# Performance work log

Measured on AMD Instinct MI355X. Metric: run time of the kernel, lower is better.

## Reference

```python
import jax, jax.numpy as jnp
import numpy as np

B, T, D, H = 16, 256, 128, 256  # batch, max_len, input_size, hidden_size (= attention hidden)


def _gru(x_seq, h0, Wih, Whh, bih, bhh):
    """Torch-style GRU over time. x_seq: [B,T,H_in], h0: [B,H]. Returns outputs [B,T,H], hT [B,H]."""
    x_proj = jnp.einsum('bti,gi->btg', x_seq, Wih) + bih  # [B,T,3H], precompute input projections

    def step(h, xp):
        gi_r, gi_z, gi_n = jnp.split(xp, 3, axis=-1)
        gh = h @ Whh.T + bhh
        gh_r, gh_z, gh_n = jnp.split(gh, 3, axis=-1)
        r = jax.nn.sigmoid(gi_r + gh_r)
        z = jax.nn.sigmoid(gi_z + gh_z)
        n = jnp.tanh(gi_n + r * gh_n)
        h_new = (1.0 - z) * n + z * h
        return h_new, h_new

    hT, outs = jax.lax.scan(step, h0, jnp.swapaxes(x_proj, 0, 1))  # scan over time
    return jnp.swapaxes(outs, 0, 1), hT


def setup_inputs() -> dict:
    key = jax.random.key(0)
    ks = jax.random.split(key, 16)
    s = lambda fan: 1.0 / np.sqrt(fan)
    inp = {
        'inputs': jax.random.normal(ks[0], (B, T, D), dtype=jnp.float32),
        'targets': jax.vmap(lambda k: jax.random.permutation(k, T))(jax.random.split(ks[1], B)).astype(jnp.int64),
        'W_enc': jax.random.normal(ks[2], (H, D), dtype=jnp.float32) * s(D),
        'b_enc': jnp.zeros((H,), dtype=jnp.float32),
        'enc_Wih': jax.random.normal(ks[3], (3 * H, H), dtype=jnp.float32) * s(H),
        'enc_Whh': jax.random.normal(ks[4], (3 * H, H), dtype=jnp.float32) * s(H),
        'enc_bih': jnp.zeros((3 * H,), dtype=jnp.float32),
        'enc_bhh': jnp.zeros((3 * H,), dtype=jnp.float32),
        'dec_Wih': jax.random.normal(ks[5], (3 * H, H), dtype=jnp.float32) * s(H),
        'dec_Whh': jax.random.normal(ks[6], (3 * H, H), dtype=jnp.float32) * s(H),
        'dec_bih': jnp.zeros((3 * H,), dtype=jnp.float32),
        'dec_bhh': jnp.zeros((3 * H,), dtype=jnp.float32),
        'Wq': jax.random.normal(ks[7], (H, H), dtype=jnp.float32) * s(H),
        'Wk': jax.random.normal(ks[8], (H, H), dtype=jnp.float32) * s(H),
        'v': jax.random.normal(ks[9], (H,), dtype=jnp.float32) * s(H),
    }
    return inp


def reference(inputs, targets, W_enc, b_enc, enc_Wih, enc_Whh, enc_bih, enc_bhh,
              dec_Wih, dec_Whh, dec_bih, dec_bhh, Wq, Wk, v):
    # encoder_linear (dropout = 0 at inference)
    enc_in = jnp.einsum('btd,hd->bth', inputs, W_enc) + b_enc  # [B,T,H]
    enc_out, hT = _gru(enc_in, jnp.zeros((B, H), dtype=inputs.dtype), enc_Wih, enc_Whh, enc_bih, enc_bhh)
    # teacher forcing: decoder inputs are encoder_inputs gathered at rolled targets
    dec_idx = jnp.roll(targets, 1, axis=1)  # [B,T]
    dec_rnn_in = jnp.take_along_axis(enc_in, dec_idx[:, :, None], axis=1)  # [B,T,H]
    dec_out, _ = _gru(dec_rnn_in, hT, dec_Wih, dec_Whh, dec_bih, dec_bhh)  # [B,T,H]
    # steps mask: position j available at step t iff j not in targets[:, :t]
    onehot = jax.nn.one_hot(targets, T, dtype=jnp.int32)         # [B,T,T]
    prev = jnp.cumsum(onehot, axis=1) - onehot                   # exclusive cumsum
    steps_mask = prev == 0                                       # [B,T(query),T(key)] bool
    # Bahdanau additive attention: v . tanh(Wq q + Wk k)
    q = jnp.einsum('bth,ah->bta', dec_out, Wq)  # [B,T,A]
    k = jnp.einsum('bsh,ah->bsa', enc_out, Wk)  # [B,S,A]
    scores = jnp.einsum('btsa,a->bts', jnp.tanh(q[:, :, None, :] + k[:, None, :, :]), v)  # [B,T,S]
    logits = jnp.where(steps_mask, scores, jnp.float32(-1e9))
    return logits
```

## Files before the change

kernel.cpp:

```cpp
#include <hip/hip_runtime.h>
#include <hip/hip_fp16.h>

#define B_ 16
#define T_ 256
#define D_ 128
#define H_ 256

typedef _Float16 f16;
typedef __attribute__((ext_vector_type(2))) _Float16 f16x2;
typedef __attribute__((ext_vector_type(4))) int i32x4;

__device__ __forceinline__ float fast_rcp(float x) {
#if __has_builtin(__builtin_amdgcn_rcpf)
    return __builtin_amdgcn_rcpf(x);
#else
    return 1.0f / x;
#endif
}
__device__ __forceinline__ float sigmoid_f(float x) {
    return fast_rcp(1.0f + __expf(-x));
}
__device__ __forceinline__ float tanh_f(float x) {
    float e = __expf(2.0f * x);
    return 1.0f - 2.0f * fast_rcp(1.0f + e);
}
__device__ __forceinline__ float tanh_pade(float x) {
    x = fminf(4.f, fmaxf(-4.f, x));
    float x2 = x * x;
    return x * (27.f + x2) * fast_rcp(27.f + 9.f * x2);
}
__device__ __forceinline__ int dot8(int a, int b, int c) {
#if __has_builtin(__builtin_amdgcn_sdot8)
    return __builtin_amdgcn_sdot8(a, b, c, false);
#else
    int d;
    asm("v_dot8_i32_i4 %0, %1, %2, %3" : "=v"(d) : "v"(a), "v"(b), "v"(c));
    return d;
#endif
}
template <int CTRL>
__device__ __forceinline__ int dpp_quad(int x) {
    return __builtin_amdgcn_update_dpp(0, x, CTRL, 0xF, 0xF, true);
}
#define DPP_XOR1 0xB1
#define DPP_XOR2 0x4E

__global__ __launch_bounds__(256) void k_wprep4(const float* __restrict__ wa,
                                                const float* __restrict__ wb,
                                                int* __restrict__ w4a, int* __restrict__ w4b,
                                                float* __restrict__ sca, float* __restrict__ scb) {
    int wid = blockIdx.x * 4 + (threadIdx.x >> 6);
    int l = threadIdx.x & 63;
    const float* W = wid < 768 ? wa : wb;
    int* w4 = wid < 768 ? w4a : w4b;
    float* sc = wid < 768 ? sca : scb;
    int r = wid & 767;
    int g = r >> 8, j = r & 255;
    const float* Wr = W + r * 256;
    float v[8];
    float m = 0.f;
    if (l < 32) {
#pragma unroll
        for (int q = 0; q < 8; ++q) {
            v[q] = Wr[8 * l + q];
            m = fmaxf(m, fabsf(v[q]));
        }
    }
#pragma unroll
    for (int d = 1; d < 64; d <<= 1) m = fmaxf(m, __shfl_xor(m, d));
    float qs = m > 0.f ? 7.f / m : 0.f;
    if (l == 0) sc[r] = m / 49.f;
    if (l < 32) {
        int pk = 0;
#pragma unroll
        for (int q = 0; q < 8; ++q) pk |= ((int)rintf(v[q] * qs) & 15) << (4 * q);
        int hf = l >> 4, i = l & 15;
        w4[(j * 2 + hf) * 48 + g * 16 + i] = pk;
    }
}

__global__ void k_pos(const int* __restrict__ tgt, int* __restrict__ pos) {
    __shared__ int pl[256];
    int b = blockIdx.x, tid = threadIdx.x;
    pl[tid] = T_;
    __syncthreads();
    atomicMin(&pl[tgt[b * 256 + tid] & 255], tid);
    __syncthreads();
    pos[b * 256 + tid] = pl[tid];
}

__global__ __launch_bounds__(256) void k_proj3(const float* __restrict__ inputs,
                                               const float* __restrict__ Wenc,
                                               const float* __restrict__ benc,
                                               const float* __restrict__ We,
                                               const float* __restrict__ bihe,
                                               const float* __restrict__ bhhe,
                                               const float* __restrict__ Wd,
                                               const float* __restrict__ bihd,
                                               const float* __restrict__ bhhd,
                                               const int* __restrict__ tgt,
                                               f16x2* __restrict__ giAe,
                                               f16* __restrict__ giBe,
                                               f16x2* __restrict__ giAd,
                                               f16* __restrict__ giBd) {
    __shared__ float s_in[16][128];
    __shared__ float s_enc[16][256];
    int blk = blockIdx.x;
    bool isdec = blk >= 256;
    int bt0 = (blk & 255) * 16;
    int b = bt0 >> 8;
    int a = threadIdx.x;
    const float* W = isdec ? Wd : We;
    const float* bih = isdec ? bihd : bihe;
    const float* bhh = isdec ? bhhd : bhhe;
    f16x2* giA = isdec ? giAd : giAe;
    f16* giB = isdec ? giBd : giBe;

    int tsrc[16];
#pragma unroll
    for (int tt = 0; tt < 16; ++tt) {
        int t = (bt0 & 255) + tt;
        tsrc[tt] = isdec ? (tgt[(b << 8) + ((t + 255) & 255)] & 255) : t;
    }
#pragma unroll
    for (int it = 0; it < 2; ++it) {
        int idx = a + it * 256;
        int row = idx >> 5, k4 = idx & 31;
        ((float4*)s_in[row])[k4] =
            *(const float4*)(inputs + (b * 256 + tsrc[row]) * 128 + k4 * 4);
    }
    __syncthreads();
    {
        float eacc[16];
#pragma unroll
        for (int tt = 0; tt < 16; ++tt) eacc[tt] = benc[a];
        const float* wr = Wenc + a * 128;
        for (int k = 0; k < 128; k += 4) {
            float4 w4 = *(const float4*)(wr + k);
#pragma unroll
            for (int tt = 0; tt < 16; ++tt) {
                float4 x4 = *(const float4*)&s_in[tt][k];
                eacc[tt] += w4.x * x4.x + w4.y * x4.y + w4.z * x4.z + w4.w * x4.w;
            }
        }
#pragma unroll
        for (int tt = 0; tt < 16; ++tt) s_enc[tt][a] = eacc[tt];
    }
    __syncthreads();
    float acc0[16], acc1[16], acc2[16];
    float b0 = bih[a] + bhh[a];
    float b1 = bih[a + 256] + bhh[a + 256];
    float b2 = bih[a + 512];
#pragma unroll
    for (int tt = 0; tt < 16; ++tt) { acc0[tt] = b0; acc1[tt] = b1; acc2[tt] = b2; }
    const float* w0 = W + a * H_;
    const float* w1 = W + (a + 256) * H_;
    const float* w2 = W + (a + 512) * H_;
    for (int k = 0; k < H_; k += 4) {
        float4 a4 = *(const float4*)(w0 + k);
        float4 b4 = *(const float4*)(w1 + k);
        float4 c4 = *(const float4*)(w2 + k);
#pragma unroll
        for (int tt = 0; tt < 16; ++tt) {
            float4 x4 = *(const float4*)&s_enc[tt][k];
            acc0[tt] += a4.x * x4.x + a4.y * x4.y + a4.z * x4.z + a4.w * x4.w;
            acc1[tt] += b4.x * x4.x + b4.y * x4.y + b4.z * x4.z + b4.w * x4.w;
            acc2[tt] += c4.x * x4.x + c4.y * x4.y + c4.z * x4.z + c4.w * x4.w;
        }
    }
#pragma unroll
    for (int tt = 0; tt < 16; ++tt) {
        int row = bt0 + tt;
        giA[row * 256 + a] = (f16x2){(f16)acc0[tt], (f16)acc1[tt]};
        giB[row * 256 + a] = (f16)acc2[tt];
    }
}

__global__ __launch_bounds__(512)
__attribute__((amdgpu_waves_per_eu(2, 2)))
void k_gru2(const int* __restrict__ w4e, const int* __restrict__ w4d,
            const float* __restrict__ sce, const float* __restrict__ scd,
            const f16x2* __restrict__ giAe, const f16* __restrict__ giBe,
            const f16x2* __restrict__ giAd, const f16* __restrict__ giBd,
            const float* __restrict__ bhhe, const float* __restrict__ bhhd,
            float* __restrict__ enc_out, float* __restrict__ dec_out) {
    __shared__ __align__(16) int sh_h4[2][32];
    const int tid = threadIdx.x;
    const int m = blockIdx.x;
    const int j = tid >> 1;
    const int hf = tid & 1;

    if (tid < 64) ((int*)sh_h4)[tid] = 0;
    float hj = 0.f;
    __syncthreads();

    for (int ph = 0; ph < 2; ++ph) {
        const int* w4 = ph ? w4d : w4e;
        const float* scp = ph ? scd : sce;
        const float sc0 = scp[j], sc1 = scp[256 + j], sc2 = scp[512 + j];
        const float bn = (ph ? bhhd : bhhe)[512 + j];
        const f16x2* gA = (ph ? giAd : giAe) + m * (T_ * 256);
        const f16* gB = (ph ? giBd : giBe) + m * (T_ * 256);
        float* outp = (ph ? dec_out : enc_out) + m * (T_ * H_);

        i32x4 wq[3][4];
        {
            unsigned long long base = (unsigned long long)(w4 + tid * 48);
#pragma unroll
            for (int g = 0; g < 3; ++g)
#pragma unroll
                for (int q4 = 0; q4 < 4; ++q4)
                    asm volatile("global_load_dwordx4 %0, %1, off offset:%2"
                                 : "=v"(wq[g][q4]) : "v"(base), "i"(g * 64 + q4 * 16));
            asm volatile("s_waitcnt vmcnt(0)" ::: "memory");
        }

        f16x2 gab = gA[j];
        f16 gn = gB[j];

        for (int t = 0; t < T_; ++t) {
            const int cur = t & 1;
            int a0 = 0, a1 = 0, a2 = 0;
            const i32x4* hb = (const i32x4*)((const char*)sh_h4 + cur * 128 + hf * 64);
#pragma unroll
            for (int q4 = 0; q4 < 4; ++q4) {
                i32x4 h4 = hb[q4];
#pragma unroll
                for (int d = 0; d < 4; ++d) {
                    a0 = dot8(wq[0][q4][d], h4[d], a0);
                    a1 = dot8(wq[1][q4][d], h4[d], a1);
                    a2 = dot8(wq[2][q4][d], h4[d], a2);
                }
            }
            const int tn = (t < T_ - 1) ? t + 1 : t;
            f16x2 ngab = gA[tn * 256 + j];
            f16 ngn = gB[tn * 256 + j];

            a0 += dpp_quad<DPP_XOR1>(a0);
            a1 += dpp_quad<DPP_XOR1>(a1);
            a2 += dpp_quad<DPP_XOR1>(a2);
            float p0 = (float)a0 * sc0;
            float p1 = (float)a1 * sc1;
            float p2 = (float)a2 * sc2;

            float rr = sigmoid_f((float)gab[0] + p0);
            float zz = sigmoid_f((float)gab[1] + p1);
            float nv = tanh_f((float)gn + rr * (p2 + bn));
            float hn = (1.f - zz) * nv + zz * hj;
            hj = hn;

            if (hf) outp[t * H_ + j] = hn;
            int nib = (int)rintf(hn * 7.f) & 15;
            int hi = dpp_quad<DPP_XOR2>(nib);
            if ((tid & 3) == 0)
                ((char*)sh_h4)[(cur ^ 1) * 128 + (tid >> 2)] = (char)(nib | (hi << 4));

            gab = ngab; gn = ngn;
            asm volatile("s_waitcnt lgkmcnt(0)" ::: "memory");
            __builtin_amdgcn_s_barrier();
        }
    }
}

__global__ __launch_bounds__(256) void k_qk(const float* __restrict__ dec_out,
                                            const float* __restrict__ Wq,
                                            const float* __restrict__ enc_out,
                                            const float* __restrict__ Wk,
                                            float* __restrict__ q,
                                            float* __restrict__ kT) {
    __shared__ float tile[8][256];
    int blk = blockIdx.x;
    bool isq = blk < 512;
    int bt0 = (isq ? blk : blk - 512) * 8;
    const float* in = isq ? dec_out : enc_out;
    const float* W = isq ? Wq : Wk;
    int a = threadIdx.x;
    float acc[8];
#pragma unroll
    for (int tt = 0; tt < 8; ++tt) acc[tt] = 0.f;
    const float* w0 = W + a * H_;
    for (int k = 0; k < H_; k += 4) {
        float4 w4 = *(const float4*)(w0 + k);
#pragma unroll
        for (int tt = 0; tt < 8; ++tt) {
            float4 x4 = *(const float4*)(in + (bt0 + tt) * H_ + k);
            acc[tt] += w4.x * x4.x + w4.y * x4.y + w4.z * x4.z + w4.w * x4.w;
        }
    }
    if (isq) {
#pragma unroll
        for (int tt = 0; tt < 8; ++tt) q[(bt0 + tt) * H_ + a] = acc[tt];
    } else {
#pragma unroll
        for (int tt = 0; tt < 8; ++tt) tile[tt][a] = acc[tt];
        __syncthreads();
        int b = bt0 >> 8, s0 = bt0 & 255;
        float4 f0 = {tile[0][a], tile[1][a], tile[2][a], tile[3][a]};
        float4 f1 = {tile[4][a], tile[5][a], tile[6][a], tile[7][a]};
        *(float4*)(kT + b * (T_ * H_) + a * T_ + s0) = f0;
        *(float4*)(kT + b * (T_ * H_) + a * T_ + s0 + 4) = f1;
    }
}

__global__ __launch_bounds__(256) void k_scores(const float* __restrict__ q,
                                                const float* __restrict__ kT,
                                                const float* __restrict__ v,
                                                const int* __restrict__ pos,
                                                float* __restrict__ out) {
    __shared__ float sq[4][256];
    __shared__ float sv[256];
    int blk = blockIdx.x;
    int b = blk >> 6;
    int t0 = (blk & 63) * 4;
    int s = threadIdx.x;
    sv[s] = v[s];
#pragma unroll
    for (int tt = 0; tt < 4; ++tt)
        sq[tt][s] = q[((b << 8) + t0 + tt) * H_ + s];
    __syncthreads();
    int ps = pos[(b << 8) + s];
    float acc[4] = {0.f, 0.f, 0.f, 0.f};
    const float* kTb = kT + b * (T_ * H_);
    for (int a = 0; a < H_; ++a) {
        float kv = kTb[a * T_ + s];
        float va = sv[a];
#pragma unroll
        for (int tt = 0; tt < 4; ++tt) {
            float th = tanh_pade(sq[tt][a] + kv);
            acc[tt] += va * th;
        }
    }
#pragma unroll
    for (int tt = 0; tt < 4; ++tt) {
        int t = t0 + tt;
        out[((b << 8) + t) * T_ + s] = (t <= ps) ? acc[tt] : -1.0e9f;
    }
}

extern "C" void kernel_launch(void* const* d_in, const int* in_sizes, int n_in,
                              void* d_out, int out_size, void* d_ws, size_t ws_size,
                              hipStream_t stream) {
    (void)in_sizes; (void)n_in; (void)out_size; (void)ws_size;
    const float* inputs   = (const float*)d_in[0];
    const int* targets    = (const int*)d_in[1];
    const float* W_enc   = (const float*)d_in[2];
    const float* b_enc   = (const float*)d_in[3];
    const float* enc_Wih = (const float*)d_in[4];
    const float* enc_Whh = (const float*)d_in[5];
    const float* enc_bih = (const float*)d_in[6];
    const float* enc_bhh = (const float*)d_in[7];
    const float* dec_Wih = (const float*)d_in[8];
    const float* dec_Whh = (const float*)d_in[9];
    const float* dec_bih = (const float*)d_in[10];
    const float* dec_bhh = (const float*)d_in[11];
    const float* Wq = (const float*)d_in[12];
    const float* Wk = (const float*)d_in[13];
    const float* v  = (const float*)d_in[14];
    float* out = (float*)d_out;

    float* ws = (float*)d_ws;
    f16x2* giAe    = (f16x2*)ws;
    f16*   giBe    = (f16*)(ws + 1048576);
    f16x2* giAd    = (f16x2*)(ws + 1572864);
    f16*   giBd    = (f16*)(ws + 2621440);
    float* enc_out = ws + 3145728;
    float* dec_out = ws + 4194304;
    int*   w4e     = (int*)(ws + 5242880);
    int*   w4d     = (int*)(ws + 5292032);
    float* sce     = ws + 5341184;
    float* scd     = ws + 5341952;
    int*   pos     = (int*)(ws + 5342720);
    float* q  = (float*)giAe;
    float* kT = (float*)giAd;

    k_wprep4<<<384, 256, 0, stream>>>(enc_Whh, dec_Whh, w4e, w4d, sce, scd);
    k_pos<<<16, 256, 0, stream>>>(targets, pos);
    k_proj3<<<512, 256, 0, stream>>>(inputs, W_enc, b_enc,
                                     enc_Wih, enc_bih, enc_bhh,
                                     dec_Wih, dec_bih, dec_bhh,
                                     targets, giAe, giBe, giAd, giBd);
    k_gru2<<<16, 512, 0, stream>>>(w4e, w4d, sce, scd, giAe, giBe, giAd, giBd,
                                   enc_bhh, dec_bhh, enc_out, dec_out);
    k_qk<<<1024, 256, 0, stream>>>(dec_out, Wq, enc_out, Wk, q, kT);
    k_scores<<<1024, 256, 0, stream>>>(q, kT, v, pos, out);
}
```

Before: 473.5 us.

## Merge prep kernels into one launch and fuse Q projection into scores

Folds weight quantization, target-position computation and input projections into a single kernel using block-index ranges, which cuts two launches. The Q projection moves into the scores kernel, so q is computed from dec_out held in shared memory and is no longer written to and read back from global memory. The K projection keeps its own kernel. The tanh clamp now uses a single med3 instruction. The cost is a larger shared-memory footprint in the scores kernel and more per-block compute there.

```diff
diff --git a/kernel.cpp b/kernel.cpp
--- a/kernel.cpp
+++ b/kernel.cpp
@@ -25,7 +25,11 @@
     return 1.0f - 2.0f * fast_rcp(1.0f + e);
 }
 __device__ __forceinline__ float tanh_pade(float x) {
+#if __has_builtin(__builtin_amdgcn_fmed3f)
+    x = __builtin_amdgcn_fmed3f(x, -4.f, 4.f);
+#else
     x = fminf(4.f, fmaxf(-4.f, x));
+#endif
     float x2 = x * x;
     return x * (27.f + x2) * fast_rcp(27.f + 9.f * x2);
 }
@@ -45,71 +49,68 @@
 #define DPP_XOR1 0xB1
 #define DPP_XOR2 0x4E
 
-__global__ __launch_bounds__(256) void k_wprep4(const float* __restrict__ wa,
-                                                const float* __restrict__ wb,
-                                                int* __restrict__ w4a, int* __restrict__ w4b,
-                                                float* __restrict__ sca, float* __restrict__ scb) {
-    int wid = blockIdx.x * 4 + (threadIdx.x >> 6);
-    int l = threadIdx.x & 63;
-    const float* W = wid < 768 ? wa : wb;
-    int* w4 = wid < 768 ? w4a : w4b;
-    float* sc = wid < 768 ? sca : scb;
-    int r = wid & 767;
-    int g = r >> 8, j = r & 255;
-    const float* Wr = W + r * 256;
-    float v[8];
-    float m = 0.f;
-    if (l < 32) {
-#pragma unroll
-        for (int q = 0; q < 8; ++q) {
-            v[q] = Wr[8 * l + q];
-            m = fmaxf(m, fabsf(v[q]));
-        }
-    }
-#pragma unroll
-    for (int d = 1; d < 64; d <<= 1) m = fmaxf(m, __shfl_xor(m, d));
-    float qs = m > 0.f ? 7.f / m : 0.f;
-    if (l == 0) sc[r] = m / 49.f;
-    if (l < 32) {
-        int pk = 0;
-#pragma unroll
-        for (int q = 0; q < 8; ++q) pk |= ((int)rintf(v[q] * qs) & 15) << (4 * q);
-        int hf = l >> 4, i = l & 15;
-        w4[(j * 2 + hf) * 48 + g * 16 + i] = pk;
-    }
-}
-
-__global__ void k_pos(const int* __restrict__ tgt, int* __restrict__ pos) {
-    __shared__ int pl[256];
-    int b = blockIdx.x, tid = threadIdx.x;
-    pl[tid] = T_;
-    __syncthreads();
-    atomicMin(&pl[tgt[b * 256 + tid] & 255], tid);
-    __syncthreads();
-    pos[b * 256 + tid] = pl[tid];
-}
-
-__global__ __launch_bounds__(256) void k_proj3(const float* __restrict__ inputs,
-                                               const float* __restrict__ Wenc,
-                                               const float* __restrict__ benc,
-                                               const float* __restrict__ We,
-                                               const float* __restrict__ bihe,
-                                               const float* __restrict__ bhhe,
-                                               const float* __restrict__ Wd,
-                                               const float* __restrict__ bihd,
-                                               const float* __restrict__ bhhd,
-                                               const int* __restrict__ tgt,
-                                               f16x2* __restrict__ giAe,
-                                               f16* __restrict__ giBe,
-                                               f16x2* __restrict__ giAd,
-                                               f16* __restrict__ giBd) {
+__global__ __launch_bounds__(256)
+void k_prep_proj(const float* __restrict__ wa, const float* __restrict__ wb,
+                 int* __restrict__ w4a, int* __restrict__ w4b,
+                 float* __restrict__ sca, float* __restrict__ scb,
+                 const int* __restrict__ tgt, int* __restrict__ pos,
+                 const float* __restrict__ inputs,
+                 const float* __restrict__ Wenc, const float* __restrict__ benc,
+                 const float* __restrict__ We, const float* __restrict__ bihe,
+                 const float* __restrict__ bhhe,
+                 const float* __restrict__ Wd, const float* __restrict__ bihd,
+                 const float* __restrict__ bhhd,
+                 f16x2* __restrict__ giAe, f16* __restrict__ giBe,
+                 f16x2* __restrict__ giAd, f16* __restrict__ giBd) {
+    int blk = blockIdx.x;
+    int a = threadIdx.x;
+    if (blk < 384) {
+        int wid = blk * 4 + (a >> 6);
+        int l = a & 63;
+        const float* W = wid < 768 ? wa : wb;
+        int* w4 = wid < 768 ? w4a : w4b;
+        float* sc = wid < 768 ? sca : scb;
+        int r = wid & 767;
+        int g = r >> 8, j = r & 255;
+        const float* Wr = W + r * 256;
+        float v[8];
+        float m = 0.f;
+        if (l < 32) {
+#pragma unroll
+            for (int q = 0; q < 8; ++q) {
+                v[q] = Wr[8 * l + q];
+                m = fmaxf(m, fabsf(v[q]));
+            }
+        }
+#pragma unroll
+        for (int d = 1; d < 64; d <<= 1) m = fmaxf(m, __shfl_xor(m, d));
+        float qs = m > 0.f ? 7.f / m : 0.f;
+        if (l == 0) sc[r] = m / 49.f;
+        if (l < 32) {
+            int pk = 0;
+#pragma unroll
+            for (int q = 0; q < 8; ++q) pk |= ((int)rintf(v[q] * qs) & 15) << (4 * q);
+            int hf = l >> 4, i = l & 15;
+            w4[(j * 2 + hf) * 48 + g * 16 + i] = pk;
+        }
+        return;
+    }
+    if (blk < 400) {
+        __shared__ int pl[256];
+        int b = blk - 384;
+        pl[a] = T_;
+        __syncthreads();
+        atomicMin(&pl[tgt[b * 256 + a] & 255], a);
+        __syncthreads();
+        pos[b * 256 + a] = pl[a];
+        return;
+    }
     __shared__ float s_in[16][128];
     __shared__ float s_enc[16][256];
-    int blk = blockIdx.x;
-    bool isdec = blk >= 256;
-    int bt0 = (blk & 255) * 16;
+    int pblk = blk - 400;
+    bool isdec = pblk >= 256;
+    int bt0 = (pblk & 255) * 16;
     int b = bt0 >> 8;
-    int a = threadIdx.x;
     const float* W = isdec ? Wd : We;
     const float* bih = isdec ? bihd : bihe;
     const float* bhh = isdec ? bhhd : bhhe;
@@ -262,51 +263,41 @@
     }
 }
 
-__global__ __launch_bounds__(256) void k_qk(const float* __restrict__ dec_out,
-                                            const float* __restrict__ Wq,
-                                            const float* __restrict__ enc_out,
+__global__ __launch_bounds__(256) void k_kT(const float* __restrict__ enc_out,
                                             const float* __restrict__ Wk,
-                                            float* __restrict__ q,
                                             float* __restrict__ kT) {
     __shared__ float tile[8][256];
-    int blk = blockIdx.x;
-    bool isq = blk < 512;
-    int bt0 = (isq ? blk : blk - 512) * 8;
-    const float* in = isq ? dec_out : enc_out;
-    const float* W = isq ? Wq : Wk;
+    int bt0 = blockIdx.x * 8;
     int a = threadIdx.x;
     float acc[8];
 #pragma unroll
     for (int tt = 0; tt < 8; ++tt) acc[tt] = 0.f;
-    const float* w0 = W + a * H_;
+    const float* w0 = Wk + a * H_;
     for (int k = 0; k < H_; k += 4) {
         float4 w4 = *(const float4*)(w0 + k);
 #pragma unroll
         for (int tt = 0; tt < 8; ++tt) {
-            float4 x4 = *(const float4*)(in + (bt0 + tt) * H_ + k);
+            float4 x4 = *(const float4*)(enc_out + (bt0 + tt) * H_ + k);
             acc[tt] += w4.x * x4.x + w4.y * x4.y + w4.z * x4.z + w4.w * x4.w;
         }
     }
-    if (isq) {
-#pragma unroll
-        for (int tt = 0; tt < 8; ++tt) q[(bt0 + tt) * H_ + a] = acc[tt];
-    } else {
-#pragma unroll
-        for (int tt = 0; tt < 8; ++tt) tile[tt][a] = acc[tt];
-        __syncthreads();
-        int b = bt0 >> 8, s0 = bt0 & 255;
-        float4 f0 = {tile[0][a], tile[1][a], tile[2][a], tile[3][a]};
-        float4 f1 = {tile[4][a], tile[5][a], tile[6][a], tile[7][a]};
-        *(float4*)(kT + b * (T_ * H_) + a * T_ + s0) = f0;
-        *(float4*)(kT + b * (T_ * H_) + a * T_ + s0 + 4) = f1;
-    }
-}
-
-__global__ __launch_bounds__(256) void k_scores(const float* __restrict__ q,
+#pragma unroll
+    for (int tt = 0; tt < 8; ++tt) tile[tt][a] = acc[tt];
+    __syncthreads();
+    int b = bt0 >> 8, s0 = bt0 & 255;
+    float4 f0 = {tile[0][a], tile[1][a], tile[2][a], tile[3][a]};
+    float4 f1 = {tile[4][a], tile[5][a], tile[6][a], tile[7][a]};
+    *(float4*)(kT + b * (T_ * H_) + a * T_ + s0) = f0;
+    *(float4*)(kT + b * (T_ * H_) + a * T_ + s0 + 4) = f1;
+}
+
+__global__ __launch_bounds__(256) void k_scores(const float* __restrict__ dec_out,
+                                                const float* __restrict__ Wq,
                                                 const float* __restrict__ kT,
                                                 const float* __restrict__ v,
                                                 const int* __restrict__ pos,
                                                 float* __restrict__ out) {
+    __shared__ float sdec[4][256];
     __shared__ float sq[4][256];
     __shared__ float sv[256];
     int blk = blockIdx.x;
@@ -316,7 +307,22 @@
     sv[s] = v[s];
 #pragma unroll
     for (int tt = 0; tt < 4; ++tt)
-        sq[tt][s] = q[((b << 8) + t0 + tt) * H_ + s];
+        sdec[tt][s] = dec_out[((b << 8) + t0 + tt) * H_ + s];
+    __syncthreads();
+    {
+        float qa[4] = {0.f, 0.f, 0.f, 0.f};
+        const float* wq = Wq + s * H_;
+        for (int k = 0; k < H_; k += 4) {
+            float4 w4 = *(const float4*)(wq + k);
+#pragma unroll
+            for (int tt = 0; tt < 4; ++tt) {
+                float4 x4 = *(const float4*)&sdec[tt][k];
+                qa[tt] += w4.x * x4.x + w4.y * x4.y + w4.z * x4.z + w4.w * x4.w;
+            }
+        }
+#pragma unroll
+        for (int tt = 0; tt < 4; ++tt) sq[tt][s] = qa[tt];
+    }
     __syncthreads();
     int ps = pos[(b << 8) + s];
     float acc[4] = {0.f, 0.f, 0.f, 0.f};
@@ -370,17 +376,15 @@
     float* sce     = ws + 5341184;
     float* scd     = ws + 5341952;
     int*   pos     = (int*)(ws + 5342720);
-    float* q  = (float*)giAe;
     float* kT = (float*)giAd;
 
-    k_wprep4<<<384, 256, 0, stream>>>(enc_Whh, dec_Whh, w4e, w4d, sce, scd);
-    k_pos<<<16, 256, 0, stream>>>(targets, pos);
-    k_proj3<<<512, 256, 0, stream>>>(inputs, W_enc, b_enc,
-                                     enc_Wih, enc_bih, enc_bhh,
-                                     dec_Wih, dec_bih, dec_bhh,
-                                     targets, giAe, giBe, giAd, giBd);
+    k_prep_proj<<<912, 256, 0, stream>>>(enc_Whh, dec_Whh, w4e, w4d, sce, scd,
+                                         targets, pos, inputs, W_enc, b_enc,
+                                         enc_Wih, enc_bih, enc_bhh,
+                                         dec_Wih, dec_bih, dec_bhh,
+                                         giAe, giBe, giAd, giBd);
     k_gru2<<<16, 512, 0, stream>>>(w4e, w4d, sce, scd, giAe, giBe, giAd, giBd,
                                    enc_bhh, dec_bhh, enc_out, dec_out);
-    k_qk<<<1024, 256, 0, stream>>>(dec_out, Wq, enc_out, Wk, q, kT);
-    k_scores<<<1024, 256, 0, stream>>>(q, kT, v, pos, out);
-}
+    k_kT<<<512, 256, 0, stream>>>(enc_out, Wk, kT);
+    k_scores<<<1024, 256, 0, stream>>>(dec_out, Wq, kT, v, pos, out);
+}
```

Measured after the change: 511.4 us. +8.0%, slower.
